# Kernel optimization log

Hardware: AMD Instinct MI355X
Metric: run time of the kernel (lower is better)

Reference implementation:

```python
import jax, jax.numpy as jnp
import numpy as np

DIM = 1024
NUM_HEADS = 16
HEAD_DIM = DIM // NUM_HEADS
SCALE = HEAD_DIM ** -0.5


def setup_inputs() -> dict:
    key = jax.random.key(0)
    ks = jax.random.split(key, 6)
    B, N, C = 2, 2048, DIM
    std = C ** -0.5
    return {
        "x_t": jax.random.normal(ks[0], (B, N, C), dtype=jnp.float32),
        "x_s": jax.random.normal(ks[1], (B, N, C), dtype=jnp.float32),
        "W_q": jax.random.normal(ks[2], (C, C), dtype=jnp.float32) * std,
        "W_kv": jax.random.normal(ks[3], (C, 2 * C), dtype=jnp.float32) * std,
        "W_fuse": jax.random.normal(ks[4], (C, C), dtype=jnp.float32) * std,
        "b_fuse": jax.random.normal(ks[5], (C,), dtype=jnp.float32) * 0.01,
    }


def reference(x_t, x_s, W_q, W_kv, W_fuse, b_fuse):
    B, N, C = x_t.shape
    H, D = NUM_HEADS, HEAD_DIM
    # q projection (no bias, qkv_bias=False): [B,N,C] -> [B,H,N,D]
    q = (x_t @ W_q).reshape(B, N, H, D).transpose(0, 2, 1, 3)
    # kv projection: [B,N,2C] -> k,v each [B,H,N,D]
    kv = (x_s @ W_kv).reshape(B, N, 2, H, D).transpose(2, 0, 3, 1, 4)
    k, v = kv[0], kv[1]
    # attention scores [B,H,N,N]
    attn = jnp.einsum("bhnd,bhmd->bhnm", q, k) * SCALE
    attn = jax.nn.softmax(attn, axis=-1)
    # weighted values -> [B,N,C]
    a = jnp.einsum("bhnm,bhmd->bhnd", attn, v).transpose(0, 2, 1, 3).reshape(B, N, C)
    # fuse projection (with bias); dropouts are identity (p=0)
    return a @ W_fuse + b_fuse
```

## Files before the change

kernel.cpp:

```cpp
#include <hip/hip_runtime.h>

#define SEQ 2048

typedef short short8 __attribute__((ext_vector_type(8)));
typedef float floatx4 __attribute__((ext_vector_type(4)));
typedef unsigned short ushort4v __attribute__((ext_vector_type(4)));
typedef unsigned int uint2v __attribute__((ext_vector_type(2)));
typedef __fp16 f16x4 __attribute__((ext_vector_type(4)));

static __device__ __forceinline__ unsigned short f2bf(float f) {
    unsigned int u = __builtin_bit_cast(unsigned int, f);
    u = (u + 0x7fffu + ((u >> 16) & 1u)) >> 16;
    return (unsigned short)u;
}

#if __has_builtin(__builtin_amdgcn_cvt_pk_bf16_f32)
typedef __bf16 bf16x2 __attribute__((ext_vector_type(2)));
static __device__ __forceinline__ unsigned int pk_bf16(float a, float b) {
    bf16x2 v = __builtin_amdgcn_cvt_pk_bf16_f32(a, b);
    return __builtin_bit_cast(unsigned int, v);
}
#else
static __device__ __forceinline__ unsigned int pk_bf16(float a, float b) {
    return (unsigned int)f2bf(a) | ((unsigned int)f2bf(b) << 16);
}
#endif

static __device__ __forceinline__ unsigned int pk_f16(float a, float b) {
    auto v = __builtin_amdgcn_cvt_pkrtz(a, b);
    return __builtin_bit_cast(unsigned int, v);
}

#define GLD16(gp, lp)                                                        \
    __builtin_amdgcn_global_load_lds(                                        \
        (const __attribute__((address_space(1))) unsigned int*)(gp),         \
        (__attribute__((address_space(3))) unsigned int*)(lp), 16, 0, 0)

__global__ void cvt2_kernel(const float4* __restrict__ a, const float4* __restrict__ b,
                            ushort4* __restrict__ oa, ushort4* __restrict__ ob, float sa) {
    int i = blockIdx.x * blockDim.x + threadIdx.x;
    if (i < 1048576) {
        float4 v = a[i];
        ushort4 o;
        o.x = f2bf(v.x * sa); o.y = f2bf(v.y * sa);
        o.z = f2bf(v.z * sa); o.w = f2bf(v.w * sa);
        oa[i] = o;
    } else {
        int j = i - 1048576;
        float4 v = b[j];
        ushort4 o;
        o.x = f2bf(v.x); o.y = f2bf(v.y);
        o.z = f2bf(v.z); o.w = f2bf(v.w);
        ob[j] = o;
    }
}

__global__ void transpose_all(const float* __restrict__ Wq, const float* __restrict__ Wkv,
                              const float* __restrict__ Wf,
                              unsigned short* __restrict__ oq, unsigned short* __restrict__ okv,
                              unsigned short* __restrict__ of_) {
    __shared__ float tile[32][33];
    int bx = blockIdx.x;
    const float* in; unsigned short* out; int N, t;
    if (bx < 1024)      { in = Wq;  out = oq;  N = 1024; t = bx; }
    else if (bx < 3072) { in = Wkv; out = okv; N = 2048; t = bx - 1024; }
    else                { in = Wf;  out = of_; N = 1024; t = bx - 3072; }
    int nb = N >> 5;
    int n0 = (t % nb) * 32, k0 = (t / nb) * 32;
    int tx = threadIdx.x, ty = threadIdx.y;
#pragma unroll
    for (int i = 0; i < 4; i++)
        tile[ty + i * 8][tx] = in[(size_t)(k0 + ty + i * 8) * N + n0 + tx];
    __syncthreads();
#pragma unroll
    for (int i = 0; i < 4; i++)
        out[(size_t)(n0 + ty + i * 8) * 1024 + k0 + tx] = f2bf(tile[tx][ty + i * 8]);
}

__global__ __launch_bounds__(256, 3)
void gemm_qkv(const unsigned short* __restrict__ xt,
              const unsigned short* __restrict__ xs,
              const unsigned short* __restrict__ wq,
              const unsigned short* __restrict__ wkv,
              unsigned short* __restrict__ q_ws,
              unsigned short* __restrict__ k_ws,
              unsigned short* __restrict__ vt_ws) {
    __shared__ unsigned short sA[128][64];
    __shared__ unsigned short sB[128][64];
    int tid = threadIdx.x, wave = tid >> 6, lane = tid & 63;
    int l15 = lane & 15, quad = lane >> 4;
    int cx = blockIdx.x;
    bool isq = cx < 8;
    const unsigned short* A  = isq ? xt : xs;
    const unsigned short* Bt = isq ? wq : wkv;
    int C0 = (isq ? cx : cx - 8) * 128;
    int R0 = blockIdx.y * 128;
    int wr = (wave >> 1) * 64, wc = (wave & 1) * 64;
    int srow = lane >> 3, scol = (lane & 7) * 8;

    floatx4 acc[4][4];
#pragma unroll
    for (int i = 0; i < 4; i++)
#pragma unroll
        for (int j = 0; j < 4; j++) acc[i][j] = (floatx4){0.f, 0.f, 0.f, 0.f};

    for (int kt = 0; kt < 16; kt++) {
        __syncthreads();
#pragma unroll
        for (int c = 0; c < 4; c++) {
            int rb = wave * 32 + c * 8;
            GLD16(&A [(size_t)(R0 + rb + srow) * 1024 + kt * 64 + scol], &sA[rb][0]);
            GLD16(&Bt[(size_t)(C0 + rb + srow) * 1024 + kt * 64 + scol], &sB[rb][0]);
        }
        __syncthreads();
#pragma unroll
        for (int ks = 0; ks < 2; ks++) {
            short8 af[4], bf[4];
#pragma unroll
            for (int mt = 0; mt < 4; mt++)
                af[mt] = *(const short8*)&sA[wr + mt * 16 + l15][ks * 32 + quad * 8];
#pragma unroll
            for (int nt = 0; nt < 4; nt++)
                bf[nt] = *(const short8*)&sB[wc + nt * 16 + l15][ks * 32 + quad * 8];
#pragma unroll
            for (int mt = 0; mt < 4; mt++)
#pragma unroll
                for (int nt = 0; nt < 4; nt++)
                    acc[mt][nt] = __builtin_amdgcn_mfma_f32_16x16x32_bf16(af[mt], bf[nt], acc[mt][nt], 0, 0, 0);
        }
    }

    int b = R0 >> 11, nb0 = (R0 & 2047) + wr;
#pragma unroll
    for (int mt = 0; mt < 4; mt++) {
#pragma unroll
        for (int nt = 0; nt < 4; nt++) {
            int col = C0 + wc + nt * 16 + l15;
            if (isq) {
                int h = col >> 6, d = col & 63;
#pragma unroll
                for (int r = 0; r < 4; r++) {
                    int n = nb0 + mt * 16 + quad * 4 + r;
                    q_ws[((size_t)((b * 16 + h) * 2048 + n)) * 64 + d] = f2bf(acc[mt][nt][r]);
                }
            } else if (col < 1024) {
                int h = col >> 6, d = col & 63;
#pragma unroll
                for (int r = 0; r < 4; r++) {
                    int n = nb0 + mt * 16 + quad * 4 + r;
                    k_ws[((size_t)((b * 16 + h) * 2048 + n)) * 64 + (d ^ ((n & 7) << 3))] = f2bf(acc[mt][nt][r]);
                }
            } else {
                int cc = col - 1024, h = cc >> 6, d = cc & 63;
                int n0 = nb0 + mt * 16 + quad * 4;
                int coln = (n0 & ~63) | ((n0 & 63) ^ ((d & 7) << 3));
                uint2v pk;
                pk.x = pk_f16(acc[mt][nt][0], acc[mt][nt][1]);
                pk.y = pk_f16(acc[mt][nt][2], acc[mt][nt][3]);
                *(uint2v*)&vt_ws[((size_t)((b * 16 + h) * 64 + d)) * 2048 + coln] = pk;
            }
        }
    }
}

__global__ __launch_bounds__(256, 3)
void gemm_fuse(const unsigned short* __restrict__ A,
               const unsigned short* __restrict__ Bt,
               float* __restrict__ out, const float* __restrict__ bias) {
    __shared__ unsigned short sA[128][64];
    __shared__ unsigned short sB[64][64];
    int tid = threadIdx.x, wave = tid >> 6, lane = tid & 63;
    int l15 = lane & 15, quad = lane >> 4;
    int R0 = blockIdx.y * 128, C0 = blockIdx.x * 64;
    int wr = (wave >> 1) * 64, wc = (wave & 1) * 32;
    int srow = lane >> 3, scol = (lane & 7) * 8;

    floatx4 acc[4][2];
#pragma unroll
    for (int i = 0; i < 4; i++)
#pragma unroll
        for (int j = 0; j < 2; j++) acc[i][j] = (floatx4){0.f, 0.f, 0.f, 0.f};

    for (int kt = 0; kt < 16; kt++) {
        __syncthreads();
#pragma unroll
        for (int c = 0; c < 4; c++) {
            int rb = wave * 32 + c * 8;
            GLD16(&A[(size_t)(R0 + rb + srow) * 1024 + kt * 64 + scol], &sA[rb][0]);
        }
#pragma unroll
        for (int c = 0; c < 2; c++) {
            int rb = wave * 16 + c * 8;
            GLD16(&Bt[(size_t)(C0 + rb + srow) * 1024 + kt * 64 + scol], &sB[rb][0]);
        }
        __syncthreads();
#pragma unroll
        for (int ks = 0; ks < 2; ks++) {
            short8 af[4], bf[2];
#pragma unroll
            for (int mt = 0; mt < 4; mt++)
                af[mt] = *(const short8*)&sA[wr + mt * 16 + l15][ks * 32 + quad * 8];
#pragma unroll
            for (int nt = 0; nt < 2; nt++)
                bf[nt] = *(const short8*)&sB[wc + nt * 16 + l15][ks * 32 + quad * 8];
#pragma unroll
            for (int mt = 0; mt < 4; mt++)
#pragma unroll
                for (int nt = 0; nt < 2; nt++)
                    acc[mt][nt] = __builtin_amdgcn_mfma_f32_16x16x32_bf16(af[mt], bf[nt], acc[mt][nt], 0, 0, 0);
        }
    }

#pragma unroll
    for (int mt = 0; mt < 4; mt++) {
#pragma unroll
        for (int r = 0; r < 4; r++) {
            int row = R0 + wr + mt * 16 + quad * 4 + r;
#pragma unroll
            for (int nt = 0; nt < 2; nt++) {
                int col = C0 + wc + nt * 16 + l15;
                out[(size_t)row * 1024 + col] = acc[mt][nt][r] + bias[col];
            }
        }
    }
}

__global__ __launch_bounds__(256, 2)
void attn_kernel(const unsigned short* __restrict__ Q,
                 const unsigned short* __restrict__ K,
                 const unsigned short* __restrict__ Vt,
                 unsigned short* __restrict__ Aout) {
    __shared__ __align__(16) unsigned short smem[16384];
    __shared__ float lred[4][4][16];

    int tid = threadIdx.x, wave = tid >> 6, lane = tid & 63;
    int l15 = lane & 15, quad = lane >> 4;
    int bh = blockIdx.y, b = bh >> 4, h = bh & 15;
    int qr0 = blockIdx.x * 64;

    const unsigned short* Qp = Q + (size_t)bh * SEQ * 64;
    const unsigned short* Kp = K + (size_t)bh * SEQ * 64;
    const unsigned short* Vp = Vt + (size_t)bh * 64 * SEQ;

    int srow = lane >> 3, scol = (lane & 7) * 8;
    int wk0 = wave * 16;

#pragma unroll
    for (int j = 0; j < 2; j++) {
        int rb = wk0 + j * 8;
        GLD16(&Kp[(size_t)(rb + srow) * 64 + scol], &smem[rb * 64]);
        GLD16(&Vp[(size_t)(rb + srow) * 2048 + scol], &smem[8192 + rb * 64]);
    }

    short8 qf[4][2];
#pragma unroll
    for (int nt = 0; nt < 4; nt++)
#pragma unroll
        for (int ks = 0; ks < 2; ks++)
            qf[nt][ks] = *(const short8*)&Qp[(size_t)(qr0 + nt * 16 + l15) * 64 + ks * 32 + quad * 8];

    floatx4 of[4][4];
#pragma unroll
    for (int i = 0; i < 4; i++)
#pragma unroll
        for (int j = 0; j < 4; j++) of[i][j] = (floatx4){0.f, 0.f, 0.f, 0.f};
    float lsum[4] = {0.f, 0.f, 0.f, 0.f};

    __syncthreads();

    int krow = wk0 + l15;
    int ksw = (l15 & 7) << 3;
    int kaddr0 = krow * 64 + ((quad * 8) ^ ksw);
    int kaddr1 = krow * 64 + ((32 + quad * 8) ^ ksw);
    int vcol = (wk0 + quad * 4) ^ ksw;

#pragma unroll 2
    for (int kt = 0; kt < 32; kt++) {
        int p = kt & 1, pb = p * 4096;
        if (kt < 31) {
            int k0n = (kt + 1) * 64;
#pragma unroll
            for (int j = 0; j < 2; j++) {
                int rb = wk0 + j * 8;
                GLD16(&Kp[(size_t)(k0n + rb + srow) * 64 + scol], &smem[(pb ^ 4096) + rb * 64]);
                GLD16(&Vp[(size_t)(rb + srow) * 2048 + k0n + scol], &smem[8192 + (pb ^ 4096) + rb * 64]);
            }
        }

        short8 kf0 = *(const short8*)&smem[pb + kaddr0];
        short8 kf1 = *(const short8*)&smem[pb + kaddr1];
        f16x4 pf[4];
#pragma unroll
        for (int nt = 0; nt < 4; nt++) {
            floatx4 zero = (floatx4){0.f, 0.f, 0.f, 0.f};
            floatx4 s = __builtin_amdgcn_mfma_f32_16x16x32_bf16(kf0, qf[nt][0], zero, 0, 0, 0);
            s = __builtin_amdgcn_mfma_f32_16x16x32_bf16(kf1, qf[nt][1], s, 0, 0, 0);
            float p0 = __builtin_amdgcn_exp2f(s[0]);
            float p1 = __builtin_amdgcn_exp2f(s[1]);
            float p2 = __builtin_amdgcn_exp2f(s[2]);
            float p3 = __builtin_amdgcn_exp2f(s[3]);
            lsum[nt] += (p0 + p1) + (p2 + p3);
            uint2v u;
            u.x = pk_f16(p0, p1);
            u.y = pk_f16(p2, p3);
            pf[nt] = __builtin_bit_cast(f16x4, u);
        }

#pragma unroll
        for (int dt = 0; dt < 4; dt++) {
            int vrow = dt * 16 + l15;
            ushort4v vv = *(const ushort4v*)&smem[8192 + pb + vrow * 64 + vcol];
            f16x4 vf = __builtin_bit_cast(f16x4, vv);
#pragma unroll
            for (int nt = 0; nt < 4; nt++)
                of[dt][nt] = __builtin_amdgcn_mfma_f32_16x16x16f16(vf, pf[nt], of[dt][nt], 0, 0, 0);
        }
        __syncthreads();
    }

#pragma unroll
    for (int nt = 0; nt < 4; nt++) {
        float l = lsum[nt];
        l += __shfl_xor(l, 16, 64);
        l += __shfl_xor(l, 32, 64);
        lsum[nt] = l;
    }
    if (quad == 0) {
#pragma unroll
        for (int nt = 0; nt < 4; nt++) lred[wave][nt][l15] = lsum[nt];
    }

    float* red = (float*)smem;

#define RED_WRITE(C, DTC)                                                          \
    _Pragma("unroll")                                                              \
    for (int nt = 0; nt < 4; nt++)                                                 \
        *(floatx4*)&red[((C) * 4 + wave) * 1024 + nt * 256 + lane * 4] = of[DTC][nt];

#define RED_STORE(DT, C, W0, W1, W2)                                               \
    {                                                                              \
        size_t obase = (size_t)(b * SEQ + qr0) * 1024 + h * 64 + (DT) * 16 + quad * 4; \
        _Pragma("unroll")                                                          \
        for (int nt = 0; nt < 4; nt++) {                                           \
            floatx4 a0 = *(const floatx4*)&red[((C) * 4 + (W0)) * 1024 + nt * 256 + lane * 4]; \
            floatx4 a1 = *(const floatx4*)&red[((C) * 4 + (W1)) * 1024 + nt * 256 + lane * 4]; \
            floatx4 a2 = *(const floatx4*)&red[((C) * 4 + (W2)) * 1024 + nt * 256 + lane * 4]; \
            floatx4 s = of[DT][nt] + a0 + a1 + a2;                                 \
            float lt = lred[0][nt][l15] + lred[1][nt][l15] + lred[2][nt][l15] + lred[3][nt][l15]; \
            float inv = 1.f / lt;                                                  \
            uint2v o;                                                              \
            o.x = pk_bf16(s[0] * inv, s[1] * inv);                                 \
            o.y = pk_bf16(s[2] * inv, s[3] * inv);                                 \
            *(uint2v*)&Aout[obase + (size_t)(nt * 16 + l15) * 1024] = o;           \
        }                                                                          \
    }

    RED_WRITE(0, 0)
    RED_WRITE(1, 1)
    __syncthreads();
    if (wave == 0)      RED_STORE(0, 0, 1, 2, 3)
    else if (wave == 1) RED_STORE(1, 1, 0, 2, 3)
    __syncthreads();
    RED_WRITE(0, 2)
    RED_WRITE(1, 3)
    __syncthreads();
    if (wave == 2)      RED_STORE(2, 0, 0, 1, 3)
    else if (wave == 3) RED_STORE(3, 1, 0, 1, 2)
#undef RED_WRITE
#undef RED_STORE
}

extern "C" void kernel_launch(void* const* d_in, const int* in_sizes, int n_in,
                              void* d_out, int out_size, void* d_ws, size_t ws_size,
                              hipStream_t stream) {
    const float* x_t  = (const float*)d_in[0];
    const float* x_s  = (const float*)d_in[1];
    const float* W_q  = (const float*)d_in[2];
    const float* W_kv = (const float*)d_in[3];
    const float* W_f  = (const float*)d_in[4];
    const float* b_f  = (const float*)d_in[5];
    float* out = (float*)d_out;

    char* ws = (char*)d_ws;
    const size_t MB = 1u << 20;
    unsigned short* xt_bf = (unsigned short*)(ws);
    unsigned short* xs_bf = (unsigned short*)(ws + 8 * MB);
    unsigned short* wq_t  = (unsigned short*)(ws + 16 * MB);
    unsigned short* wkv_t = (unsigned short*)(ws + 18 * MB);
    unsigned short* wf_t  = (unsigned short*)(ws + 22 * MB);
    unsigned short* q_ws  = (unsigned short*)(ws + 24 * MB);
    unsigned short* k_ws  = (unsigned short*)(ws + 32 * MB);
    unsigned short* vt_ws = (unsigned short*)(ws + 40 * MB);
    unsigned short* a_ws  = (unsigned short*)(ws + 48 * MB);

    cvt2_kernel<<<8192, 256, 0, stream>>>((const float4*)x_t, (const float4*)x_s,
                                          (ushort4*)xt_bf, (ushort4*)xs_bf,
                                          0.125f * 1.44269504088896340736f);
    transpose_all<<<4096, dim3(32, 8), 0, stream>>>(W_q, W_kv, W_f, wq_t, wkv_t, wf_t);

    gemm_qkv<<<dim3(24, 32), 256, 0, stream>>>(xt_bf, xs_bf, wq_t, wkv_t, q_ws, k_ws, vt_ws);
    attn_kernel<<<dim3(32, 32), 256, 0, stream>>>(q_ws, k_ws, vt_ws, a_ws);
    gemm_fuse<<<dim3(16, 32), 256, 0, stream>>>(a_ws, wf_t, out, b_f);
}
```

Baseline: 214.4 us.

## Restructure attention K/V pipeline with explicit waitcnt, priority, and XCD-aware block remap

Rewrites the attention main loop to prefetch two K/V tiles up front and issue the next-next tile load after compute, using explicit s_waitcnt vmcnt and raw s_barrier instead of __syncthreads so loads overlap compute better. Adds s_setprio around the MFMA/exp section. Remaps the 1D grid so consecutive blocks on the same XCD work on the same (batch,head), with the aim of improving L2 reuse of K/V. The hand-placed waitcnt counts and barriers are fragile and rely on the GLD16 issue count matching vmcnt(4).

New measurement: 213.9 us. No clear change (-0.2%).

```diff
diff --git a/kernel.cpp b/kernel.cpp
--- a/kernel.cpp
+++ b/kernel.cpp
@@ -235,8 +235,12 @@
 
     int tid = threadIdx.x, wave = tid >> 6, lane = tid & 63;
     int l15 = lane & 15, quad = lane >> 4;
-    int bh = blockIdx.y, b = bh >> 4, h = bh & 15;
-    int qr0 = blockIdx.x * 64;
+
+    int id = blockIdx.x;
+    int logical = (id & 7) * 128 + (id >> 3);
+    int bh = logical >> 5, qt = logical & 31;
+    int b = bh >> 4, h = bh & 15;
+    int qr0 = qt * 64;
 
     const unsigned short* Qp = Q + (size_t)bh * SEQ * 64;
     const unsigned short* Kp = K + (size_t)bh * SEQ * 64;
@@ -245,11 +249,16 @@
     int srow = lane >> 3, scol = (lane & 7) * 8;
     int wk0 = wave * 16;
 
-#pragma unroll
-    for (int j = 0; j < 2; j++) {
-        int rb = wk0 + j * 8;
-        GLD16(&Kp[(size_t)(rb + srow) * 64 + scol], &smem[rb * 64]);
-        GLD16(&Vp[(size_t)(rb + srow) * 2048 + scol], &smem[8192 + rb * 64]);
+#define STAGE(tile, pbase)                                                    \
+    {                                                                         \
+        _Pragma("unroll")                                                     \
+        for (int j = 0; j < 2; j++) {                                         \
+            int rb = wk0 + j * 8;                                             \
+            GLD16(&Kp[(size_t)((tile) * 64 + rb + srow) * 64 + scol],         \
+                  &smem[(pbase) + rb * 64]);                                  \
+            GLD16(&Vp[(size_t)(rb + srow) * 2048 + (tile) * 64 + scol],       \
+                  &smem[8192 + (pbase) + rb * 64]);                           \
+        }                                                                     \
     }
 
     short8 qf[4][2];
@@ -259,14 +268,15 @@
         for (int ks = 0; ks < 2; ks++)
             qf[nt][ks] = *(const short8*)&Qp[(size_t)(qr0 + nt * 16 + l15) * 64 + ks * 32 + quad * 8];
 
+    STAGE(0, 0)
+    STAGE(1, 4096)
+
     floatx4 of[4][4];
 #pragma unroll
     for (int i = 0; i < 4; i++)
 #pragma unroll
         for (int j = 0; j < 4; j++) of[i][j] = (floatx4){0.f, 0.f, 0.f, 0.f};
     float lsum[4] = {0.f, 0.f, 0.f, 0.f};
-
-    __syncthreads();
 
     int krow = wk0 + l15;
     int ksw = (l15 & 7) << 3;
@@ -274,19 +284,11 @@
     int kaddr1 = krow * 64 + ((32 + quad * 8) ^ ksw);
     int vcol = (wk0 + quad * 4) ^ ksw;
 
-#pragma unroll 2
-    for (int kt = 0; kt < 32; kt++) {
-        int p = kt & 1, pb = p * 4096;
-        if (kt < 31) {
-            int k0n = (kt + 1) * 64;
-#pragma unroll
-            for (int j = 0; j < 2; j++) {
-                int rb = wk0 + j * 8;
-                GLD16(&Kp[(size_t)(k0n + rb + srow) * 64 + scol], &smem[(pb ^ 4096) + rb * 64]);
-                GLD16(&Vp[(size_t)(rb + srow) * 2048 + k0n + scol], &smem[8192 + (pb ^ 4096) + rb * 64]);
-            }
-        }
-
+    asm volatile("s_waitcnt vmcnt(0)" ::: "memory");
+    __syncthreads();
+
+    auto compute = [&](int pb) {
+        __builtin_amdgcn_s_setprio(1);
         short8 kf0 = *(const short8*)&smem[pb + kaddr0];
         short8 kf1 = *(const short8*)&smem[pb + kaddr1];
         f16x4 pf[4];
@@ -305,7 +307,6 @@
             u.y = pk_f16(p2, p3);
             pf[nt] = __builtin_bit_cast(f16x4, u);
         }
-
 #pragma unroll
         for (int dt = 0; dt < 4; dt++) {
             int vrow = dt * 16 + l15;
@@ -315,8 +316,25 @@
             for (int nt = 0; nt < 4; nt++)
                 of[dt][nt] = __builtin_amdgcn_mfma_f32_16x16x16f16(vf, pf[nt], of[dt][nt], 0, 0, 0);
         }
-        __syncthreads();
-    }
+        __builtin_amdgcn_s_setprio(0);
+    };
+
+#pragma unroll 2
+    for (int kt = 0; kt < 30; kt++) {
+        int pb = (kt & 1) * 4096;
+        compute(pb);
+        __builtin_amdgcn_sched_barrier(0);
+        asm volatile("s_barrier" ::: "memory");
+        STAGE(kt + 2, pb)
+        asm volatile("s_waitcnt vmcnt(4)" ::: "memory");
+        asm volatile("s_barrier" ::: "memory");
+        __builtin_amdgcn_sched_barrier(0);
+    }
+    compute(0);
+    asm volatile("s_waitcnt vmcnt(0)" ::: "memory");
+    asm volatile("s_barrier" ::: "memory");
+    compute(4096);
+#undef STAGE
 
 #pragma unroll
     for (int nt = 0; nt < 4; nt++) {
@@ -329,6 +347,7 @@
 #pragma unroll
         for (int nt = 0; nt < 4; nt++) lred[wave][nt][l15] = lsum[nt];
     }
+    __syncthreads();
 
     float* red = (float*)smem;
 
@@ -399,6 +418,6 @@
     transpose_all<<<4096, dim3(32, 8), 0, stream>>>(W_q, W_kv, W_f, wq_t, wkv_t, wf_t);
 
     gemm_qkv<<<dim3(24, 32), 256, 0, stream>>>(xt_bf, xs_bf, wq_t, wkv_t, q_ws, k_ws, vt_ws);
-    attn_kernel<<<dim3(32, 32), 256, 0, stream>>>(q_ws, k_ws, vt_ws, a_ws);
+    attn_kernel<<<1024, 256, 0, stream>>>(q_ws, k_ws, vt_ws, a_ws);
     gemm_fuse<<<dim3(16, 32), 256, 0, stream>>>(a_ws, wf_t, out, b_f);
 }
```

## Load K/V fragments directly from global into registers, dropping LDS staging

Applied to the files above, without the earlier changes.

The attention kernel no longer stages K and V tiles through shared memory. Each wave now loads its own K and V^T fragments straight from global memory into registers, software-pipelined two key tiles ahead, and the per-iteration __syncthreads goes away. It processes two key tiles per step so it can use the wider 16x16x32 f16 MFMA for PV, raises wave priority around the compute, and remaps the grid to a 1D launch with a swizzled block order for L2 locality. The QKV GEMM epilogue drops the XOR swizzle on K/V^T writes, since LDS bank conflicts no longer apply. The trade-off is more register pressure and uncoalesced-ish global reads in place of shared-memory reuse.

After: 268.8 us. +25.3%, slower.

```diff
diff --git a/kernel.cpp b/kernel.cpp
--- a/kernel.cpp
+++ b/kernel.cpp
@@ -4,9 +4,9 @@
 
 typedef short short8 __attribute__((ext_vector_type(8)));
 typedef float floatx4 __attribute__((ext_vector_type(4)));
-typedef unsigned short ushort4v __attribute__((ext_vector_type(4)));
 typedef unsigned int uint2v __attribute__((ext_vector_type(2)));
-typedef __fp16 f16x4 __attribute__((ext_vector_type(4)));
+typedef unsigned int uint4v __attribute__((ext_vector_type(4)));
+typedef __fp16 f16x8 __attribute__((ext_vector_type(8)));
 
 static __device__ __forceinline__ unsigned short f2bf(float f) {
     unsigned int u = __builtin_bit_cast(unsigned int, f);
@@ -148,16 +148,15 @@
 #pragma unroll
                 for (int r = 0; r < 4; r++) {
                     int n = nb0 + mt * 16 + quad * 4 + r;
-                    k_ws[((size_t)((b * 16 + h) * 2048 + n)) * 64 + (d ^ ((n & 7) << 3))] = f2bf(acc[mt][nt][r]);
+                    k_ws[((size_t)((b * 16 + h) * 2048 + n)) * 64 + d] = f2bf(acc[mt][nt][r]);
                 }
             } else {
                 int cc = col - 1024, h = cc >> 6, d = cc & 63;
-                int n0 = nb0 + mt * 16 + quad * 4;
-                int coln = (n0 & ~63) | ((n0 & 63) ^ ((d & 7) << 3));
+                int n = nb0 + mt * 16 + quad * 4;
                 uint2v pk;
                 pk.x = pk_f16(acc[mt][nt][0], acc[mt][nt][1]);
                 pk.y = pk_f16(acc[mt][nt][2], acc[mt][nt][3]);
-                *(uint2v*)&vt_ws[((size_t)((b * 16 + h) * 64 + d)) * 2048 + coln] = pk;
+                *(uint2v*)&vt_ws[((size_t)((b * 16 + h) * 64 + d)) * 2048 + n] = pk;
             }
         }
     }
@@ -235,22 +234,18 @@
 
     int tid = threadIdx.x, wave = tid >> 6, lane = tid & 63;
     int l15 = lane & 15, quad = lane >> 4;
-    int bh = blockIdx.y, b = bh >> 4, h = bh & 15;
-    int qr0 = blockIdx.x * 64;
+
+    int id = blockIdx.x;
+    int logical = (id & 7) * 128 + (id >> 3);
+    int bh = logical >> 5, qt = logical & 31;
+    int b = bh >> 4, h = bh & 15;
+    int qr0 = qt * 64;
 
     const unsigned short* Qp = Q + (size_t)bh * SEQ * 64;
     const unsigned short* Kp = K + (size_t)bh * SEQ * 64;
     const unsigned short* Vp = Vt + (size_t)bh * 64 * SEQ;
 
-    int srow = lane >> 3, scol = (lane & 7) * 8;
     int wk0 = wave * 16;
-
-#pragma unroll
-    for (int j = 0; j < 2; j++) {
-        int rb = wk0 + j * 8;
-        GLD16(&Kp[(size_t)(rb + srow) * 64 + scol], &smem[rb * 64]);
-        GLD16(&Vp[(size_t)(rb + srow) * 2048 + scol], &smem[8192 + rb * 64]);
-    }
 
     short8 qf[4][2];
 #pragma unroll
@@ -259,6 +254,13 @@
         for (int ks = 0; ks < 2; ks++)
             qf[nt][ks] = *(const short8*)&Qp[(size_t)(qr0 + nt * 16 + l15) * 64 + ks * 32 + quad * 8];
 
+    auto loadK = [&](int tile, int ks) {
+        return *(const short8*)&Kp[(size_t)(tile * 64 + wk0 + l15) * 64 + ks * 32 + quad * 8];
+    };
+    auto loadV = [&](int tile, int dt) {
+        return *(const uint2v*)&Vp[(size_t)(dt * 16 + l15) * 2048 + tile * 64 + wk0 + quad * 4];
+    };
+
     floatx4 of[4][4];
 #pragma unroll
     for (int i = 0; i < 4; i++)
@@ -266,56 +268,67 @@
         for (int j = 0; j < 4; j++) of[i][j] = (floatx4){0.f, 0.f, 0.f, 0.f};
     float lsum[4] = {0.f, 0.f, 0.f, 0.f};
 
-    __syncthreads();
-
-    int krow = wk0 + l15;
-    int ksw = (l15 & 7) << 3;
-    int kaddr0 = krow * 64 + ((quad * 8) ^ ksw);
-    int kaddr1 = krow * 64 + ((32 + quad * 8) ^ ksw);
-    int vcol = (wk0 + quad * 4) ^ ksw;
+    short8 kc[4]; uint2v vc[8];
+    kc[0] = loadK(0, 0); kc[1] = loadK(0, 1); kc[2] = loadK(1, 0); kc[3] = loadK(1, 1);
+#pragma unroll
+    for (int dt = 0; dt < 4; dt++) { vc[dt * 2] = loadV(0, dt); vc[dt * 2 + 1] = loadV(1, dt); }
 
 #pragma unroll 2
-    for (int kt = 0; kt < 32; kt++) {
-        int p = kt & 1, pb = p * 4096;
-        if (kt < 31) {
-            int k0n = (kt + 1) * 64;
-#pragma unroll
-            for (int j = 0; j < 2; j++) {
-                int rb = wk0 + j * 8;
-                GLD16(&Kp[(size_t)(k0n + rb + srow) * 64 + scol], &smem[(pb ^ 4096) + rb * 64]);
-                GLD16(&Vp[(size_t)(rb + srow) * 2048 + k0n + scol], &smem[8192 + (pb ^ 4096) + rb * 64]);
-            }
-        }
-
-        short8 kf0 = *(const short8*)&smem[pb + kaddr0];
-        short8 kf1 = *(const short8*)&smem[pb + kaddr1];
-        f16x4 pf[4];
+    for (int p = 0; p < 16; p++) {
+        short8 kn[4]; uint2v vn[8];
+        if (p < 15) {
+            int tA = 2 * p + 2, tB = 2 * p + 3;
+            kn[0] = loadK(tA, 0); kn[1] = loadK(tA, 1);
+            kn[2] = loadK(tB, 0); kn[3] = loadK(tB, 1);
+#pragma unroll
+            for (int dt = 0; dt < 4; dt++) { vn[dt * 2] = loadV(tA, dt); vn[dt * 2 + 1] = loadV(tB, dt); }
+        }
+
+        __builtin_amdgcn_s_setprio(1);
+        uint2v pka[4], pkb[4];
 #pragma unroll
         for (int nt = 0; nt < 4; nt++) {
-            floatx4 zero = (floatx4){0.f, 0.f, 0.f, 0.f};
-            floatx4 s = __builtin_amdgcn_mfma_f32_16x16x32_bf16(kf0, qf[nt][0], zero, 0, 0, 0);
-            s = __builtin_amdgcn_mfma_f32_16x16x32_bf16(kf1, qf[nt][1], s, 0, 0, 0);
+            floatx4 z = (floatx4){0.f, 0.f, 0.f, 0.f};
+            floatx4 s = __builtin_amdgcn_mfma_f32_16x16x32_bf16(kc[0], qf[nt][0], z, 0, 0, 0);
+            s = __builtin_amdgcn_mfma_f32_16x16x32_bf16(kc[1], qf[nt][1], s, 0, 0, 0);
             float p0 = __builtin_amdgcn_exp2f(s[0]);
             float p1 = __builtin_amdgcn_exp2f(s[1]);
             float p2 = __builtin_amdgcn_exp2f(s[2]);
             float p3 = __builtin_amdgcn_exp2f(s[3]);
             lsum[nt] += (p0 + p1) + (p2 + p3);
-            uint2v u;
-            u.x = pk_f16(p0, p1);
-            u.y = pk_f16(p2, p3);
-            pf[nt] = __builtin_bit_cast(f16x4, u);
-        }
-
+            pka[nt].x = pk_f16(p0, p1); pka[nt].y = pk_f16(p2, p3);
+        }
+#pragma unroll
+        for (int nt = 0; nt < 4; nt++) {
+            floatx4 z = (floatx4){0.f, 0.f, 0.f, 0.f};
+            floatx4 s = __builtin_amdgcn_mfma_f32_16x16x32_bf16(kc[2], qf[nt][0], z, 0, 0, 0);
+            s = __builtin_amdgcn_mfma_f32_16x16x32_bf16(kc[3], qf[nt][1], s, 0, 0, 0);
+            float p0 = __builtin_amdgcn_exp2f(s[0]);
+            float p1 = __builtin_amdgcn_exp2f(s[1]);
+            float p2 = __builtin_amdgcn_exp2f(s[2]);
+            float p3 = __builtin_amdgcn_exp2f(s[3]);
+            lsum[nt] += (p0 + p1) + (p2 + p3);
+            pkb[nt].x = pk_f16(p0, p1); pkb[nt].y = pk_f16(p2, p3);
+        }
 #pragma unroll
         for (int dt = 0; dt < 4; dt++) {
-            int vrow = dt * 16 + l15;
-            ushort4v vv = *(const ushort4v*)&smem[8192 + pb + vrow * 64 + vcol];
-            f16x4 vf = __builtin_bit_cast(f16x4, vv);
-#pragma unroll
-            for (int nt = 0; nt < 4; nt++)
-                of[dt][nt] = __builtin_amdgcn_mfma_f32_16x16x16f16(vf, pf[nt], of[dt][nt], 0, 0, 0);
-        }
-        __syncthreads();
+            f16x8 vf = __builtin_bit_cast(f16x8,
+                (uint4v){vc[2 * dt].x, vc[2 * dt].y, vc[2 * dt + 1].x, vc[2 * dt + 1].y});
+#pragma unroll
+            for (int nt = 0; nt < 4; nt++) {
+                f16x8 pf = __builtin_bit_cast(f16x8,
+                    (uint4v){pka[nt].x, pka[nt].y, pkb[nt].x, pkb[nt].y});
+                of[dt][nt] = __builtin_amdgcn_mfma_f32_16x16x32_f16(vf, pf, of[dt][nt], 0, 0, 0);
+            }
+        }
+        __builtin_amdgcn_s_setprio(0);
+
+        if (p < 15) {
+#pragma unroll
+            for (int i = 0; i < 4; i++) kc[i] = kn[i];
+#pragma unroll
+            for (int i = 0; i < 8; i++) vc[i] = vn[i];
+        }
     }
 
 #pragma unroll
@@ -329,6 +342,7 @@
 #pragma unroll
         for (int nt = 0; nt < 4; nt++) lred[wave][nt][l15] = lsum[nt];
     }
+    __syncthreads();
 
     float* red = (float*)smem;
 
@@ -399,6 +413,6 @@
     transpose_all<<<4096, dim3(32, 8), 0, stream>>>(W_q, W_kv, W_f, wq_t, wkv_t, wf_t);
 
     gemm_qkv<<<dim3(24, 32), 256, 0, stream>>>(xt_bf, xs_bf, wq_t, wkv_t, q_ws, k_ws, vt_ws);
-    attn_kernel<<<dim3(32, 32), 256, 0, stream>>>(q_ws, k_ws, vt_ws, a_ws);
+    attn_kernel<<<1024, 256, 0, stream>>>(q_ws, k_ws, vt_ws, a_ws);
     gemm_fuse<<<dim3(16, 32), 256, 0, stream>>>(a_ws, wf_t, out, b_f);
 }
```
